# Kernel tuning notes

Measured on AMD Instinct MI355X. Metric: run time of the kernel, lower is better.

## Reference

```python
import jax, jax.numpy as jnp
import numpy as np

TEMPERATURE = 0.07


def setup_inputs() -> dict:
    key = jax.random.key(0)
    k1, k2, k3 = jax.random.split(key, 3)
    b, num_proposals, num_phrases, f = 128, 100, 16, 512
    img_features = jax.random.normal(k1, (b, num_proposals, f), dtype=jnp.float32)
    text_features = jax.random.normal(k2, (b, num_phrases, f), dtype=jnp.float32)
    labels = jax.random.randint(k3, (b, b), 0, 2, dtype=jnp.int64)
    return {"img_features": img_features, "text_features": text_features, "labels": labels}


def reference(img_features, text_features, labels):
    # att_matrix[b,d,t,i] = <text[b,t,:], img[d,i,:]>
    att_matrix = jnp.einsum('btf,dif->bdti', text_features, img_features)
    argmax_box = att_matrix.max(axis=3)        # [b, d, t]  max over proposals
    score_matrix = argmax_box.mean(axis=2)     # [b, d]     mean over phrases
    score_exp = jnp.exp(score_matrix / TEMPERATURE)
    return score_exp
```

## Files before the change

kernel.cpp:

```cpp
#include <hip/hip_runtime.h>
#include <hip/hip_bf16.h>
#include <stdint.h>


typedef __attribute__((ext_vector_type(4))) int   v4i;
typedef __attribute__((ext_vector_type(8))) int   v8i;
typedef __attribute__((ext_vector_type(4))) float f32x4;

constexpr int Bb = 128;
constexpr int P  = 100;
constexpr int T  = 16;
constexpr int F  = 512;
constexpr float TEMP = 0.07f;

constexpr int BM = 128;
constexpr int BK = 128;
constexpr int NK = F / BK;

__global__ void cvt_kernel(const float4* __restrict__ img, const float4* __restrict__ txt,
                           uint32_t* __restrict__ imgb, uint32_t* __restrict__ txtb,
                           int nimg4, int ntxt4) {
  const int stride = gridDim.x * blockDim.x;
  for (int i = blockIdx.x * blockDim.x + threadIdx.x; i < nimg4; i += stride) {
    float4 v = img[i];
    int w = __builtin_amdgcn_cvt_pk_fp8_f32(v.x, v.y, 0, false);
    w     = __builtin_amdgcn_cvt_pk_fp8_f32(v.z, v.w, w, true);
    imgb[i] = (uint32_t)w;
  }
  for (int i = blockIdx.x * blockDim.x + threadIdx.x; i < ntxt4; i += stride) {
    float4 v = txt[i];
    int w = __builtin_amdgcn_cvt_pk_fp8_f32(v.x, v.y, 0, false);
    w     = __builtin_amdgcn_cvt_pk_fp8_f32(v.z, v.w, w, true);
    txtb[i] = (uint32_t)w;
  }
}

template<bool FUSED>
__global__ __launch_bounds__(256)
void score_kernel(const void* __restrict__ imgp, const void* __restrict__ txtp,
                  float* __restrict__ out) {
  __shared__ __align__(16) unsigned char As[2][BM * BK];
  __shared__ __align__(16) unsigned char Bs[2][BM * BK];
  __shared__ float red[BM][2];

  const int d    = blockIdx.x;
  const int b0   = blockIdx.y * (BM / T);
  const int tid  = threadIdx.x;
  const int lane = tid & 63;
  const int w    = tid >> 6;
  const int q    = lane >> 4;
  const int n    = lane & 15;
  const int mh   = w & 1;
  const int nh   = w >> 1;

  f32x4 acc[4][4] = {};

  auto stage = [&](int buf, int kk) {
    if constexpr (!FUSED) {
      const uint8_t* gi = (const uint8_t*)imgp;
      const uint8_t* gt = (const uint8_t*)txtp;
      const int sub = lane >> 3;
      const int col = (((lane & 7) ^ sub) & 7) * 16;
      #pragma unroll
      for (int rr = 0; rr < 4; rr++) {
        const int c   = rr * 4 + w;
        const int row = c * 8 + sub;
        const uint8_t* ga = gt + (size_t)(b0 * T + row) * F + kk + col;
        __builtin_amdgcn_global_load_lds(
            (const __attribute__((address_space(1))) void*)ga,
            (__attribute__((address_space(3))) void*)&As[buf][c * 1024], 16, 0, 0);
        const int prow = row < P ? row : 0;
        const uint8_t* gb = gi + ((size_t)d * P + prow) * F + kk + col;
        __builtin_amdgcn_global_load_lds(
            (const __attribute__((address_space(1))) void*)gb,
            (__attribute__((address_space(3))) void*)&Bs[buf][c * 1024], 16, 0, 0);
      }
    } else {
      const float* gi = (const float*)imgp;
      const float* gt = (const float*)txtp;
      #pragma unroll
      for (int s = 0; s < 8; s++) {
        const int slot = s * 256 + tid;
        const int row  = slot >> 4;
        const int half = slot & 15;
        const int colf = half * 8;
        const int swz  = ((half >> 1) ^ (row & 7));
        const int offb = row * BK + swz * 16 + (half & 1) * 8;
        float4 v0 = *(const float4*)(gt + (size_t)(b0 * T + row) * F + kk + colf);
        float4 v1 = *(const float4*)(gt + (size_t)(b0 * T + row) * F + kk + colf + 4);
        int w0 = __builtin_amdgcn_cvt_pk_fp8_f32(v0.x, v0.y, 0, false);
        w0     = __builtin_amdgcn_cvt_pk_fp8_f32(v0.z, v0.w, w0, true);
        int w1 = __builtin_amdgcn_cvt_pk_fp8_f32(v1.x, v1.y, 0, false);
        w1     = __builtin_amdgcn_cvt_pk_fp8_f32(v1.z, v1.w, w1, true);
        *(uint2*)&As[buf][offb] = make_uint2((uint32_t)w0, (uint32_t)w1);
        const int prow = row < P ? row : 0;
        float4 u0 = *(const float4*)(gi + ((size_t)d * P + prow) * F + kk + colf);
        float4 u1 = *(const float4*)(gi + ((size_t)d * P + prow) * F + kk + colf + 4);
        int x0 = __builtin_amdgcn_cvt_pk_fp8_f32(u0.x, u0.y, 0, false);
        x0     = __builtin_amdgcn_cvt_pk_fp8_f32(u0.z, u0.w, x0, true);
        int x1 = __builtin_amdgcn_cvt_pk_fp8_f32(u1.x, u1.y, 0, false);
        x1     = __builtin_amdgcn_cvt_pk_fp8_f32(u1.z, u1.w, x1, true);
        *(uint2*)&Bs[buf][offb] = make_uint2((uint32_t)x0, (uint32_t)x1);
      }
    }
  };

  stage(0, 0);

  #pragma unroll
  for (int k4 = 0; k4 < NK; k4++) {
    __syncthreads();
    if (k4 + 1 < NK) stage((k4 + 1) & 1, (k4 + 1) * BK);

    const unsigned char* Ab = As[k4 & 1];
    const unsigned char* Bbuf = Bs[k4 & 1];
    const int k7 = n & 7;
    const int s0 = (2 * q) ^ k7;
    v8i a[4], bfr[4];
    #pragma unroll
    for (int rt = 0; rt < 4; rt++) {
      const int off = (mh * 64 + rt * 16 + n) * BK;
      v4i lo = *(const v4i*)&Ab[off + s0 * 16];
      v4i hi = *(const v4i*)&Ab[off + (s0 ^ 1) * 16];
      a[rt] = __builtin_shufflevector(lo, hi, 0, 1, 2, 3, 4, 5, 6, 7);
    }
    #pragma unroll
    for (int ct = 0; ct < 4; ct++) {
      const int off = (nh * 64 + ct * 16 + n) * BK;
      v4i lo = *(const v4i*)&Bbuf[off + s0 * 16];
      v4i hi = *(const v4i*)&Bbuf[off + (s0 ^ 1) * 16];
      bfr[ct] = __builtin_shufflevector(lo, hi, 0, 1, 2, 3, 4, 5, 6, 7);
    }
    #pragma unroll
    for (int rt = 0; rt < 4; rt++)
      #pragma unroll
      for (int ct = 0; ct < 4; ct++)
        acc[rt][ct] = __builtin_amdgcn_mfma_scale_f32_16x16x128_f8f6f4(
            a[rt], bfr[ct], acc[rt][ct], 0, 0, 0, 127, 0, 127);
  }

  #pragma unroll
  for (int rt = 0; rt < 4; rt++) {
    float m[4];
    #pragma unroll
    for (int r = 0; r < 4; r++) {
      float v = -3.0e38f;
      #pragma unroll
      for (int ct = 0; ct < 4; ct++) {
        const bool valid = (nh * 64 + ct * 16 + n) < P;
        const float x = acc[rt][ct][r];
        v = valid ? fmaxf(v, x) : v;
      }
      #pragma unroll
      for (int off = 1; off < 16; off <<= 1)
        v = fmaxf(v, __shfl_xor(v, off));
      m[r] = v;
    }
    if (n == 0) {
      #pragma unroll
      for (int r = 0; r < 4; r++)
        red[mh * 64 + rt * 16 + q * 4 + r][nh] = m[r];
    }
  }
  __syncthreads();

  if (tid < BM / T) {
    float s = 0.f;
    #pragma unroll
    for (int t = 0; t < T; t++) {
      const int r = tid * T + t;
      s += fmaxf(red[r][0], red[r][1]);
    }
    const float arg = fminf(s * (1.0f / (T * TEMP)), 88.0f);
    out[(size_t)(b0 + tid) * Bb + d] = expf(arg);
  }
}

extern "C" void kernel_launch(void* const* d_in, const int* in_sizes, int n_in,
                              void* d_out, int out_size, void* d_ws, size_t ws_size,
                              hipStream_t stream) {
  const float* img = (const float*)d_in[0];
  const float* txt = (const float*)d_in[1];
  float* out = (float*)d_out;

  const size_t imgN = (size_t)Bb * P * F;
  const size_t txtN = (size_t)Bb * T * F;
  const size_t need = imgN + txtN;

  dim3 grid(Bb, (Bb * T) / BM);
  if (ws_size >= need) {
    uint8_t* imgb = (uint8_t*)d_ws;
    uint8_t* txtb = imgb + imgN;
    cvt_kernel<<<2048, 256, 0, stream>>>((const float4*)img, (const float4*)txt,
                                         (uint32_t*)imgb, (uint32_t*)txtb,
                                         (int)(imgN / 4), (int)(txtN / 4));
    score_kernel<false><<<grid, 256, 0, stream>>>(imgb, txtb, out);
  } else {
    score_kernel<true><<<grid, 256, 0, stream>>>(img, txt, out);
  }
}
```

Measured before the change: 102.2 us.

## Single-buffer LDS, raise occupancy target, interleave B-fragment loads with MFMA

Drops LDS double buffering, cutting shared memory per block from 64KB to 32KB, and requests four blocks per CU in the launch bounds. This should let more blocks co-reside and hide latency through occupancy rather than software prefetch. B fragments are now loaded one column tile at a time just before their MFMAs, which lowers register pressure, and s_setprio raises wave priority around each MFMA group. The cost is an extra barrier per K step and no overlap between global loads and compute inside a block.

```diff
diff --git a/kernel.cpp b/kernel.cpp
--- a/kernel.cpp
+++ b/kernel.cpp
@@ -36,11 +36,11 @@
 }
 
 template<bool FUSED>
-__global__ __launch_bounds__(256)
+__global__ __launch_bounds__(256, 4)
 void score_kernel(const void* __restrict__ imgp, const void* __restrict__ txtp,
                   float* __restrict__ out) {
-  __shared__ __align__(16) unsigned char As[2][BM * BK];
-  __shared__ __align__(16) unsigned char Bs[2][BM * BK];
+  __shared__ __align__(16) unsigned char As[BM * BK];
+  __shared__ __align__(16) unsigned char Bs[BM * BK];
   __shared__ float red[BM][2];
 
   const int d    = blockIdx.x;
@@ -55,7 +55,7 @@
 
   f32x4 acc[4][4] = {};
 
-  auto stage = [&](int buf, int kk) {
+  auto stage = [&](int kk) {
     if constexpr (!FUSED) {
       const uint8_t* gi = (const uint8_t*)imgp;
       const uint8_t* gt = (const uint8_t*)txtp;
@@ -68,12 +68,12 @@
         const uint8_t* ga = gt + (size_t)(b0 * T + row) * F + kk + col;
         __builtin_amdgcn_global_load_lds(
             (const __attribute__((address_space(1))) void*)ga,
-            (__attribute__((address_space(3))) void*)&As[buf][c * 1024], 16, 0, 0);
+            (__attribute__((address_space(3))) void*)&As[c * 1024], 16, 0, 0);
         const int prow = row < P ? row : 0;
         const uint8_t* gb = gi + ((size_t)d * P + prow) * F + kk + col;
         __builtin_amdgcn_global_load_lds(
             (const __attribute__((address_space(1))) void*)gb,
-            (__attribute__((address_space(3))) void*)&Bs[buf][c * 1024], 16, 0, 0);
+            (__attribute__((address_space(3))) void*)&Bs[c * 1024], 16, 0, 0);
       }
     } else {
       const float* gi = (const float*)imgp;
@@ -92,7 +92,7 @@
         w0     = __builtin_amdgcn_cvt_pk_fp8_f32(v0.z, v0.w, w0, true);
         int w1 = __builtin_amdgcn_cvt_pk_fp8_f32(v1.x, v1.y, 0, false);
         w1     = __builtin_amdgcn_cvt_pk_fp8_f32(v1.z, v1.w, w1, true);
-        *(uint2*)&As[buf][offb] = make_uint2((uint32_t)w0, (uint32_t)w1);
+        *(uint2*)&As[offb] = make_uint2((uint32_t)w0, (uint32_t)w1);
         const int prow = row < P ? row : 0;
         float4 u0 = *(const float4*)(gi + ((size_t)d * P + prow) * F + kk + colf);
         float4 u1 = *(const float4*)(gi + ((size_t)d * P + prow) * F + kk + colf + 4);
@@ -100,43 +100,41 @@
         x0     = __builtin_amdgcn_cvt_pk_fp8_f32(u0.z, u0.w, x0, true);
         int x1 = __builtin_amdgcn_cvt_pk_fp8_f32(u1.x, u1.y, 0, false);
         x1     = __builtin_amdgcn_cvt_pk_fp8_f32(u1.z, u1.w, x1, true);
-        *(uint2*)&Bs[buf][offb] = make_uint2((uint32_t)x0, (uint32_t)x1);
+        *(uint2*)&Bs[offb] = make_uint2((uint32_t)x0, (uint32_t)x1);
       }
     }
   };
 
-  stage(0, 0);
+  const int s0 = (2 * q) ^ (n & 7);
 
   #pragma unroll
   for (int k4 = 0; k4 < NK; k4++) {
+    stage(k4 * BK);
     __syncthreads();
-    if (k4 + 1 < NK) stage((k4 + 1) & 1, (k4 + 1) * BK);
 
-    const unsigned char* Ab = As[k4 & 1];
-    const unsigned char* Bbuf = Bs[k4 & 1];
-    const int k7 = n & 7;
-    const int s0 = (2 * q) ^ k7;
-    v8i a[4], bfr[4];
+    v8i a[4];
     #pragma unroll
     for (int rt = 0; rt < 4; rt++) {
       const int off = (mh * 64 + rt * 16 + n) * BK;
-      v4i lo = *(const v4i*)&Ab[off + s0 * 16];
-      v4i hi = *(const v4i*)&Ab[off + (s0 ^ 1) * 16];
+      v4i lo = *(const v4i*)&As[off + s0 * 16];
+      v4i hi = *(const v4i*)&As[off + (s0 ^ 1) * 16];
       a[rt] = __builtin_shufflevector(lo, hi, 0, 1, 2, 3, 4, 5, 6, 7);
     }
     #pragma unroll
     for (int ct = 0; ct < 4; ct++) {
       const int off = (nh * 64 + ct * 16 + n) * BK;
-      v4i lo = *(const v4i*)&Bbuf[off + s0 * 16];
-      v4i hi = *(const v4i*)&Bbuf[off + (s0 ^ 1) * 16];
-      bfr[ct] = __builtin_shufflevector(lo, hi, 0, 1, 2, 3, 4, 5, 6, 7);
+      v4i lo = *(const v4i*)&Bs[off + s0 * 16];
+      v4i hi = *(const v4i*)&Bs[off + (s0 ^ 1) * 16];
+      v8i bfr = __builtin_shufflevector(lo, hi, 0, 1, 2, 3, 4, 5, 6, 7);
+      __builtin_amdgcn_s_setprio(1);
+      #pragma unroll
+      for (int rt = 0; rt < 4; rt++)
+        acc[rt][ct] = __builtin_amdgcn_mfma_scale_f32_16x16x128_f8f6f4(
+            a[rt], bfr, acc[rt][ct], 0, 0, 0, 127, 0, 127);
+      __builtin_amdgcn_s_setprio(0);
     }
-    #pragma unroll
-    for (int rt = 0; rt < 4; rt++)
-      #pragma unroll
-      for (int ct = 0; ct < 4; ct++)
-        acc[rt][ct] = __builtin_amdgcn_mfma_scale_f32_16x16x128_f8f6f4(
-            a[rt], bfr[ct], acc[rt][ct], 0, 0, 0, 127, 0, 127);
+
+    if (k4 + 1 < NK) __syncthreads();
   }
 
   #pragma unroll
```

Measured after the change: 142.1 us. 39.0% more time.
